# Kernel tuning notes

Measured on AMD Instinct MI355X. Metric: run time of the kernel, lower is better.

The kernel has to match this reference:

```python
import jax, jax.numpy as jnp
import numpy as np

B, S, ENC, DEC, ATTN = 64, 2048, 512, 512, 256

def setup_inputs() -> dict:
    key = jax.random.key(0)
    k1, k2, k3, k4, k5 = jax.random.split(key, 5)
    s = 0.05
    return {
        "enc_outputs": jax.random.normal(k1, (B, S, ENC), dtype=jnp.float32),
        "dec_state": jax.random.normal(k2, (B, DEC), dtype=jnp.float32),
        "W_enc": jax.random.normal(k3, (ENC, ATTN), dtype=jnp.float32) * s,
        "W_dec": jax.random.normal(k4, (DEC, ATTN), dtype=jnp.float32) * s,
        "v": jax.random.normal(k5, (ATTN,), dtype=jnp.float32) * s,
    }

def reference(enc_outputs, dec_state, W_enc, W_dec, v):
    # enc_proj: [B,S,A], dec_proj: [B,1,A]
    enc_proj = jnp.einsum('bse,ea->bsa', enc_outputs, W_enc)
    dec_proj = jnp.einsum('bd,da->ba', dec_state, W_dec)[:, None, :]
    scores = jnp.einsum('bsa,a->bs', jnp.tanh(enc_proj + dec_proj), v)  # [B,S]
    attn_weights = jax.nn.softmax(scores, axis=-1)
    context = jnp.einsum('bs,bse->be', attn_weights, enc_outputs)  # [B,ENC]
    return (context, attn_weights)
```

## Files before the change

kernel.cpp:

```cpp
#include <hip/hip_runtime.h>
#include <hip/hip_bf16.h>
#include <stdint.h>

#define B_    64
#define S_    2048
#define ENC_  512
#define ATTN_ 256

typedef __bf16 bf16;
typedef bf16  bf16x8 __attribute__((ext_vector_type(8)));
typedef float f32x4  __attribute__((ext_vector_type(4)));

__device__ __forceinline__ float fexp2(float x) {
#if __has_builtin(__builtin_amdgcn_exp2f)
    return __builtin_amdgcn_exp2f(x);
#else
    return exp2f(x);
#endif
}
__device__ __forceinline__ float frcp(float x) {
#if __has_builtin(__builtin_amdgcn_rcpf)
    return __builtin_amdgcn_rcpf(x);
#else
    return 1.0f / x;
#endif
}
__device__ __forceinline__ float fast_tanh(float x) {
    float e = fexp2(x * 2.8853900817779268f);
    return 1.0f - 2.0f * frcp(e + 1.0f);
}

__device__ __forceinline__ void async_copy16(const void* g, void* l) {
#if __has_builtin(__builtin_amdgcn_global_load_lds)
    __builtin_amdgcn_global_load_lds(
        (__attribute__((address_space(1))) void*)(g),
        (__attribute__((address_space(3))) void*)(l), 16, 0, 0);
#else
    *(uint4*)l = *(const uint4*)g;
#endif
}

__global__ __launch_bounds__(256) void k_setup(const float* __restrict__ W_enc,
                                               const float* __restrict__ dec_state,
                                               const float* __restrict__ W_dec,
                                               bf16* __restrict__ WT,
                                               float* __restrict__ dp,
                                               float* __restrict__ ctx) {
    int blk = blockIdx.x;
    if (blk < 512) {
        int idx = blk * 256 + threadIdx.x;
        int n = idx >> 9;
        int k = idx & 511;
        WT[idx] = (bf16)W_enc[k * ATTN_ + n];
    } else {
        int b = blk - 512;
        int a = threadIdx.x;
        *(float2*)(ctx + b * 512 + a * 2) = make_float2(0.f, 0.f);
        const float* ds = dec_state + b * 512;
        float acc = 0.f;
#pragma unroll 8
        for (int d = 0; d < 512; ++d)
            acc += ds[d] * W_dec[d * ATTN_ + a];
        dp[b * ATTN_ + a] = acc;
    }
}

__device__ __forceinline__ void stage_b(const bf16* __restrict__ WT, bf16* bsbuf,
                                        int ks, int bcol4, int bslot, int tid) {
#pragma unroll
    for (int r = 0; r < 4; ++r) {
        int c = r * 64 + bcol4;
        int g = bslot ^ ((c + (c >> 2)) & 3);
        async_copy16(WT + (size_t)c * 512 + ks * 32 + g * 8,
                     bsbuf + r * 2048 + tid * 8);
    }
}

__global__ __launch_bounds__(256, 2) void k_scores(
    const float* __restrict__ enc,
    const bf16*  __restrict__ WT,
    const float* __restrict__ dp,
    const float* __restrict__ v,
    float* __restrict__ out_scores)
{
    __shared__ __align__(16) bf16 As[2][128 * 40];
    __shared__ __align__(16) bf16 Bs[2][256 * 32];
    __shared__ float partial[4][64];

    const int tid  = threadIdx.x;
    const int wave = tid >> 6;
    const int lane = tid & 63;
    const int l15  = lane & 15;
    const int q    = lane >> 4;
    const int m0   = blockIdx.x * 128;
    const int b    = blockIdx.x >> 4;

    const int mrow0 = (wave >> 1) * 64;
    const int ncol0 = (wave & 1) * 128;

    const f32x4 zero4 = {0.f, 0.f, 0.f, 0.f};
    f32x4 acc[4][8];
#pragma unroll
    for (int mt = 0; mt < 4; ++mt)
#pragma unroll
        for (int nt = 0; nt < 8; ++nt)
            acc[mt][nt] = zero4;

    const int arow = tid >> 1;
    const int akc  = tid & 1;
    const float* ag = enc + (size_t)(m0 + arow) * 512 + akc * 16;
    const int aoff = arow * 40 + akc * 16;

    const int bcol4 = tid >> 2;
    const int bslot = tid & 3;

    {
        float4 f0 = *(const float4*)(ag);
        float4 f1 = *(const float4*)(ag + 4);
        float4 f2 = *(const float4*)(ag + 8);
        float4 f3 = *(const float4*)(ag + 12);
        stage_b(WT, Bs[0], 0, bcol4, bslot, tid);
        bf16x8 lo, hi;
        lo[0]=(bf16)f0.x; lo[1]=(bf16)f0.y; lo[2]=(bf16)f0.z; lo[3]=(bf16)f0.w;
        lo[4]=(bf16)f1.x; lo[5]=(bf16)f1.y; lo[6]=(bf16)f1.z; lo[7]=(bf16)f1.w;
        hi[0]=(bf16)f2.x; hi[1]=(bf16)f2.y; hi[2]=(bf16)f2.z; hi[3]=(bf16)f2.w;
        hi[4]=(bf16)f3.x; hi[5]=(bf16)f3.y; hi[6]=(bf16)f3.z; hi[7]=(bf16)f3.w;
        *(bf16x8*)(&As[0][aoff])     = lo;
        *(bf16x8*)(&As[0][aoff + 8]) = hi;
    }
    __syncthreads();

    for (int ks = 0; ks < 16; ++ks) {
        const int cur = ks & 1;
        const bf16* Asc = As[cur];
        const bf16* Bsc = Bs[cur];

        bf16x8 af[4];
#pragma unroll
        for (int mt = 0; mt < 4; ++mt) {
            int row = mrow0 + mt * 16 + l15;
            af[mt] = *(const bf16x8*)(Asc + row * 40 + q * 8);
        }
        bf16x8 bfr[8];
#pragma unroll
        for (int nt = 0; nt < 8; ++nt) {
            int col = ncol0 + nt * 16 + l15;
            int p = q ^ ((col + (col >> 2)) & 3);
            bfr[nt] = *(const bf16x8*)(Bsc + col * 32 + p * 8);
        }

        float4 f0, f1, f2, f3;
        if (ks < 15) {
            const float* s = ag + (ks + 1) * 32;
            f0 = *(const float4*)(s);
            f1 = *(const float4*)(s + 4);
            f2 = *(const float4*)(s + 8);
            f3 = *(const float4*)(s + 12);
            stage_b(WT, Bs[cur ^ 1], ks + 1, bcol4, bslot, tid);
        }

#pragma unroll
        for (int mt = 0; mt < 4; ++mt)
#pragma unroll
            for (int nt = 0; nt < 8; ++nt)
                acc[mt][nt] = __builtin_amdgcn_mfma_f32_16x16x32_bf16(af[mt], bfr[nt], acc[mt][nt], 0, 0, 0);

        if (ks < 15) {
            bf16x8 lo, hi;
            lo[0]=(bf16)f0.x; lo[1]=(bf16)f0.y; lo[2]=(bf16)f0.z; lo[3]=(bf16)f0.w;
            lo[4]=(bf16)f1.x; lo[5]=(bf16)f1.y; lo[6]=(bf16)f1.z; lo[7]=(bf16)f1.w;
            hi[0]=(bf16)f2.x; hi[1]=(bf16)f2.y; hi[2]=(bf16)f2.z; hi[3]=(bf16)f2.w;
            hi[4]=(bf16)f3.x; hi[5]=(bf16)f3.y; hi[6]=(bf16)f3.z; hi[7]=(bf16)f3.w;
            bf16* dst = &As[cur ^ 1][aoff];
            *(bf16x8*)(dst)     = lo;
            *(bf16x8*)(dst + 8) = hi;
        }
        __syncthreads();
    }

    float dpv[8], vv[8];
#pragma unroll
    for (int nt = 0; nt < 8; ++nt) {
        int col = ncol0 + nt * 16 + l15;
        dpv[nt] = dp[b * 256 + col];
        vv[nt]  = v[col];
    }
#pragma unroll
    for (int mt = 0; mt < 4; ++mt) {
#pragma unroll
        for (int r = 0; r < 4; ++r) {
            float s = 0.f;
#pragma unroll
            for (int nt = 0; nt < 8; ++nt)
                s += fast_tanh(acc[mt][nt][r] + dpv[nt]) * vv[nt];
            s += __shfl_xor(s, 1, 16);
            s += __shfl_xor(s, 2, 16);
            s += __shfl_xor(s, 4, 16);
            s += __shfl_xor(s, 8, 16);
            if (l15 == 0)
                partial[wave][mt * 16 + q * 4 + r] = s;
        }
    }
    __syncthreads();
    if (tid < 128) {
        int mw   = tid >> 6;
        int rloc = tid & 63;
        out_scores[m0 + mw * 64 + rloc] =
            partial[mw * 2][rloc] + partial[mw * 2 + 1][rloc];
    }
}

__global__ __launch_bounds__(256) void k_ctx(const float* __restrict__ enc,
                                             const float* __restrict__ scores,
                                             float* __restrict__ attn,
                                             float* __restrict__ ctx) {
    __shared__ float red[256];
    __shared__ float wlds[128];
    __shared__ f32x4 vred[128];

    const int tid  = threadIdx.x;
    const int b    = blockIdx.x >> 4;
    const int slab = blockIdx.x & 15;
    const float* sc = scores + b * 2048;

    float x[8];
    float mx = -1e30f;
#pragma unroll
    for (int i = 0; i < 8; ++i) { x[i] = sc[tid + 256 * i]; mx = fmaxf(mx, x[i]); }
    red[tid] = mx;
    __syncthreads();
    for (int off = 128; off > 0; off >>= 1) {
        if (tid < off) red[tid] = fmaxf(red[tid], red[tid + off]);
        __syncthreads();
    }
    mx = red[0];
    __syncthreads();

    float e[8];
    float lsum = 0.f;
#pragma unroll
    for (int i = 0; i < 8; ++i) { e[i] = fexp2((x[i] - mx) * 1.4426950408889634f); lsum += e[i]; }
    red[tid] = lsum;
    __syncthreads();
    for (int off = 128; off > 0; off >>= 1) {
        if (tid < off) red[tid] += red[tid + off];
        __syncthreads();
    }
    float inv = 1.0f / red[0];

#pragma unroll
    for (int i = 0; i < 8; ++i) {
        int idx = tid + 256 * i;
        int r   = idx - slab * 128;
        if ((unsigned)r < 128u) {
            float w = e[i] * inv;
            attn[b * 2048 + idx] = w;
            wlds[r] = w;
        }
    }
    __syncthreads();

    const int eq = tid & 127;
    const int sr = tid >> 7;
    const float* eb = enc + ((size_t)b * 2048 + slab * 128) * 512;

    f32x4 acc = {0.f, 0.f, 0.f, 0.f};
    for (int g = 0; g < 8; ++g) {
        const int sbase = g * 16 + sr * 8;
        f32x4 ev[8];
        float wv[8];
#pragma unroll
        for (int j = 0; j < 8; ++j) {
            ev[j] = *(const f32x4*)(eb + (size_t)(sbase + j) * 512 + eq * 4);
            wv[j] = wlds[sbase + j];
        }
#pragma unroll
        for (int j = 0; j < 8; ++j) acc += ev[j] * wv[j];
    }
    if (sr) vred[eq] = acc;
    __syncthreads();
    if (!sr) {
        acc += vred[eq];
        float* cp = ctx + b * 512 + eq * 4;
        atomicAdd(cp + 0, acc[0]);
        atomicAdd(cp + 1, acc[1]);
        atomicAdd(cp + 2, acc[2]);
        atomicAdd(cp + 3, acc[3]);
    }
}

extern "C" void kernel_launch(void* const* d_in, const int* in_sizes, int n_in,
                              void* d_out, int out_size, void* d_ws, size_t ws_size,
                              hipStream_t stream) {
    const float* enc       = (const float*)d_in[0];
    const float* dec_state = (const float*)d_in[1];
    const float* W_enc     = (const float*)d_in[2];
    const float* W_dec     = (const float*)d_in[3];
    const float* v         = (const float*)d_in[4];

    float* ctx  = (float*)d_out;
    float* attn = (float*)d_out + 64 * 512;

    char*  ws     = (char*)d_ws;
    bf16*  WT     = (bf16*)ws;
    float* dp     = (float*)(ws + 256 * 1024);
    float* scores = (float*)(ws + 256 * 1024 + 64 * 1024);

    k_setup <<<576, 256, 0, stream>>>(W_enc, dec_state, W_dec, WT, dp, ctx);
    k_scores<<<1024, 256, 0, stream>>>(enc, WT, dp, v, scores);
    k_ctx   <<<1024, 256, 0, stream>>>(enc, scores, attn, ctx);
}
```

Before: 446.7 us.

## Deepen A-tile prefetch in scores GEMM and restructure context kernel softmax/loads

```diff
diff --git a/kernel.cpp b/kernel.cpp
--- a/kernel.cpp
+++ b/kernel.cpp
@@ -76,6 +76,25 @@
     }
 }
 
+__device__ __forceinline__ void load_a4(const float* s, float4& f0, float4& f1,
+                                        float4& f2, float4& f3) {
+    f0 = *(const float4*)(s);
+    f1 = *(const float4*)(s + 4);
+    f2 = *(const float4*)(s + 8);
+    f3 = *(const float4*)(s + 12);
+}
+
+__device__ __forceinline__ void cvt_store(bf16* dst, float4 f0, float4 f1,
+                                          float4 f2, float4 f3) {
+    bf16x8 lo, hi;
+    lo[0]=(bf16)f0.x; lo[1]=(bf16)f0.y; lo[2]=(bf16)f0.z; lo[3]=(bf16)f0.w;
+    lo[4]=(bf16)f1.x; lo[5]=(bf16)f1.y; lo[6]=(bf16)f1.z; lo[7]=(bf16)f1.w;
+    hi[0]=(bf16)f2.x; hi[1]=(bf16)f2.y; hi[2]=(bf16)f2.z; hi[3]=(bf16)f2.w;
+    hi[4]=(bf16)f3.x; hi[5]=(bf16)f3.y; hi[6]=(bf16)f3.z; hi[7]=(bf16)f3.w;
+    *(bf16x8*)(dst)     = lo;
+    *(bf16x8*)(dst + 8) = hi;
+}
+
 __global__ __launch_bounds__(256, 2) void k_scores(
     const float* __restrict__ enc,
     const bf16*  __restrict__ WT,
@@ -114,22 +133,16 @@
     const int bcol4 = tid >> 2;
     const int bslot = tid & 3;
 
-    {
-        float4 f0 = *(const float4*)(ag);
-        float4 f1 = *(const float4*)(ag + 4);
-        float4 f2 = *(const float4*)(ag + 8);
-        float4 f3 = *(const float4*)(ag + 12);
-        stage_b(WT, Bs[0], 0, bcol4, bslot, tid);
-        bf16x8 lo, hi;
-        lo[0]=(bf16)f0.x; lo[1]=(bf16)f0.y; lo[2]=(bf16)f0.z; lo[3]=(bf16)f0.w;
-        lo[4]=(bf16)f1.x; lo[5]=(bf16)f1.y; lo[6]=(bf16)f1.z; lo[7]=(bf16)f1.w;
-        hi[0]=(bf16)f2.x; hi[1]=(bf16)f2.y; hi[2]=(bf16)f2.z; hi[3]=(bf16)f2.w;
-        hi[4]=(bf16)f3.x; hi[5]=(bf16)f3.y; hi[6]=(bf16)f3.z; hi[7]=(bf16)f3.w;
-        *(bf16x8*)(&As[0][aoff])     = lo;
-        *(bf16x8*)(&As[0][aoff + 8]) = hi;
-    }
-    __syncthreads();
-
+    float4 xa0, xa1, xa2, xa3;
+    float4 ya0, ya1, ya2, ya3;
+
+    load_a4(ag,      xa0, xa1, xa2, xa3);
+    load_a4(ag + 32, ya0, ya1, ya2, ya3);
+    stage_b(WT, Bs[0], 0, bcol4, bslot, tid);
+    cvt_store(&As[0][aoff], xa0, xa1, xa2, xa3);
+    __syncthreads();
+
+#pragma unroll
     for (int ks = 0; ks < 16; ++ks) {
         const int cur = ks & 1;
         const bf16* Asc = As[cur];
@@ -149,14 +162,11 @@
             bfr[nt] = *(const bf16x8*)(Bsc + col * 32 + p * 8);
         }
 
-        float4 f0, f1, f2, f3;
-        if (ks < 15) {
-            const float* s = ag + (ks + 1) * 32;
-            f0 = *(const float4*)(s);
-            f1 = *(const float4*)(s + 4);
-            f2 = *(const float4*)(s + 8);
-            f3 = *(const float4*)(s + 12);
-            stage_b(WT, Bs[cur ^ 1], ks + 1, bcol4, bslot, tid);
+        if (ks < 15) stage_b(WT, Bs[cur ^ 1], ks + 1, bcol4, bslot, tid);
+        if (ks < 14) {
+            const float* s = ag + (ks + 2) * 32;
+            if ((ks & 1) == 0) load_a4(s, xa0, xa1, xa2, xa3);
+            else               load_a4(s, ya0, ya1, ya2, ya3);
         }
 
 #pragma unroll
@@ -166,14 +176,9 @@
                 acc[mt][nt] = __builtin_amdgcn_mfma_f32_16x16x32_bf16(af[mt], bfr[nt], acc[mt][nt], 0, 0, 0);
 
         if (ks < 15) {
-            bf16x8 lo, hi;
-            lo[0]=(bf16)f0.x; lo[1]=(bf16)f0.y; lo[2]=(bf16)f0.z; lo[3]=(bf16)f0.w;
-            lo[4]=(bf16)f1.x; lo[5]=(bf16)f1.y; lo[6]=(bf16)f1.z; lo[7]=(bf16)f1.w;
-            hi[0]=(bf16)f2.x; hi[1]=(bf16)f2.y; hi[2]=(bf16)f2.z; hi[3]=(bf16)f2.w;
-            hi[4]=(bf16)f3.x; hi[5]=(bf16)f3.y; hi[6]=(bf16)f3.z; hi[7]=(bf16)f3.w;
             bf16* dst = &As[cur ^ 1][aoff];
-            *(bf16x8*)(dst)     = lo;
-            *(bf16x8*)(dst + 8) = hi;
+            if ((ks & 1) == 0) cvt_store(dst, ya0, ya1, ya2, ya3);
+            else               cvt_store(dst, xa0, xa1, xa2, xa3);
         }
         __syncthreads();
     }
@@ -214,45 +219,51 @@
                                              const float* __restrict__ scores,
                                              float* __restrict__ attn,
                                              float* __restrict__ ctx) {
-    __shared__ float red[256];
-    __shared__ float wlds[128];
+    __shared__ float redm[4], reds[4];
+    __shared__ float wlds[64];
     __shared__ f32x4 vred[128];
 
     const int tid  = threadIdx.x;
-    const int b    = blockIdx.x >> 4;
-    const int slab = blockIdx.x & 15;
+    const int wave = tid >> 6;
+    const int lane = tid & 63;
+    const int b    = blockIdx.x >> 5;
+    const int slab = blockIdx.x & 31;
     const float* sc = scores + b * 2048;
+
+    const int eq = tid & 127;
+    const int sr = tid >> 7;
+    const float* eb = enc + ((size_t)b * 2048 + slab * 64) * 512;
+
+    f32x4 ev0[8];
+#pragma unroll
+    for (int j = 0; j < 8; ++j)
+        ev0[j] = *(const f32x4*)(eb + (size_t)(sr * 8 + j) * 512 + eq * 4);
 
     float x[8];
     float mx = -1e30f;
 #pragma unroll
     for (int i = 0; i < 8; ++i) { x[i] = sc[tid + 256 * i]; mx = fmaxf(mx, x[i]); }
-    red[tid] = mx;
-    __syncthreads();
-    for (int off = 128; off > 0; off >>= 1) {
-        if (tid < off) red[tid] = fmaxf(red[tid], red[tid + off]);
-        __syncthreads();
-    }
-    mx = red[0];
-    __syncthreads();
+#pragma unroll
+    for (int d = 1; d < 64; d <<= 1) mx = fmaxf(mx, __shfl_xor(mx, d));
+    if (lane == 0) redm[wave] = mx;
+    __syncthreads();
+    mx = fmaxf(fmaxf(redm[0], redm[1]), fmaxf(redm[2], redm[3]));
 
     float e[8];
     float lsum = 0.f;
 #pragma unroll
     for (int i = 0; i < 8; ++i) { e[i] = fexp2((x[i] - mx) * 1.4426950408889634f); lsum += e[i]; }
-    red[tid] = lsum;
-    __syncthreads();
-    for (int off = 128; off > 0; off >>= 1) {
-        if (tid < off) red[tid] += red[tid + off];
-        __syncthreads();
-    }
-    float inv = 1.0f / red[0];
+#pragma unroll
+    for (int d = 1; d < 64; d <<= 1) lsum += __shfl_xor(lsum, d);
+    if (lane == 0) reds[wave] = lsum;
+    __syncthreads();
+    float inv = 1.0f / (reds[0] + reds[1] + reds[2] + reds[3]);
 
 #pragma unroll
     for (int i = 0; i < 8; ++i) {
         int idx = tid + 256 * i;
-        int r   = idx - slab * 128;
-        if ((unsigned)r < 128u) {
+        int r   = idx - slab * 64;
+        if ((unsigned)r < 64u) {
             float w = e[i] * inv;
             attn[b * 2048 + idx] = w;
             wlds[r] = w;
@@ -260,12 +271,11 @@
     }
     __syncthreads();
 
-    const int eq = tid & 127;
-    const int sr = tid >> 7;
-    const float* eb = enc + ((size_t)b * 2048 + slab * 128) * 512;
-
     f32x4 acc = {0.f, 0.f, 0.f, 0.f};
-    for (int g = 0; g < 8; ++g) {
+#pragma unroll
+    for (int j = 0; j < 8; ++j) acc += ev0[j] * wlds[sr * 8 + j];
+
+    for (int g = 1; g < 4; ++g) {
         const int sbase = g * 16 + sr * 8;
         f32x4 ev[8];
         float wv[8];
@@ -308,5 +318,5 @@
 
     k_setup <<<576, 256, 0, stream>>>(W_enc, dec_state, W_dec, WT, dp, ctx);
     k_scores<<<1024, 256, 0, stream>>>(enc, WT, dp, v, scores);
-    k_ctx   <<<1024, 256, 0, stream>>>(enc, scores, attn, ctx);
-}
+    k_ctx   <<<2048, 256, 0, stream>>>(enc, scores, attn, ctx);
+}
```

New measurement: 449.2 us. About the same (+0.6%).
